# Optimization experiments

Measured on AMD Instinct MI355X. Metric: run time of the kernel, lower is better.

## Reference

```python
import jax, jax.numpy as jnp
import numpy as np

N_NODES = 100000
N_EDGES = 3200000
D_IN, D_HID, D_OUT = 256, 256, 256
B, V, C = 64, 50, 64
DEC_H1, DEC_H2, N_CLS = 512, 256, 1000
NEG_INF = -1e9


def setup_inputs() -> dict:
    key = jax.random.key(0)
    ks = jax.random.split(key, 20)
    s = lambda d: 1.0 / np.sqrt(d)
    return {
        'edge_index': jax.random.randint(ks[0], (2, N_EDGES), 0, N_NODES, dtype=jnp.int64 if jax.config.jax_enable_x64 else jnp.int32),
        'edge_weight': jax.random.uniform(ks[1], (N_EDGES,), dtype=jnp.float32),
        'codes_x': jax.random.randint(ks[2], (B, V, C), 0, N_NODES, dtype=jnp.int64 if jax.config.jax_enable_x64 else jnp.int32),
        'node_emb': jax.random.normal(ks[3], (N_NODES, D_IN), jnp.float32) * 0.02,
        'W1': jax.random.normal(ks[4], (D_IN, D_HID), jnp.float32) * s(D_IN),
        'b1': jnp.zeros((D_HID,), jnp.float32),
        'W2': jax.random.normal(ks[5], (D_HID, D_OUT), jnp.float32) * s(D_HID),
        'b2': jnp.zeros((D_OUT,), jnp.float32),
        'Wv': jax.random.normal(ks[6], (D_OUT, D_OUT), jnp.float32) * s(D_OUT),
        'uv': jax.random.normal(ks[7], (D_OUT,), jnp.float32) * s(D_OUT),
        'Wp': jax.random.normal(ks[8], (D_OUT, D_OUT), jnp.float32) * s(D_OUT),
        'up': jax.random.normal(ks[9], (D_OUT,), jnp.float32) * s(D_OUT),
        'Wd1': jax.random.normal(ks[10], (D_OUT, DEC_H1), jnp.float32) * s(D_OUT),
        'bd1': jnp.zeros((DEC_H1,), jnp.float32),
        'Wd2': jax.random.normal(ks[11], (DEC_H1, DEC_H2), jnp.float32) * s(DEC_H1),
        'bd2': jnp.zeros((DEC_H2,), jnp.float32),
        'Wd3': jax.random.normal(ks[12], (DEC_H2, N_CLS), jnp.float32) * s(DEC_H2),
        'bd3': jnp.zeros((N_CLS,), jnp.float32),
    }


def reference(edge_index, edge_weight, codes_x, node_emb, W1, b1, W2, b2,
              Wv, uv, Wp, up, Wd1, bd1, Wd2, bd2, Wd3, bd3):
    n = node_emb.shape[0]
    src, dst = edge_index[0], edge_index[1]

    def agg(x):  # weighted message passing: out_i = sum_{e: dst=i} w_e * x[src_e]
        return jax.ops.segment_sum(x[src] * edge_weight[:, None], dst, num_segments=n)

    # 2-layer weighted GCN over the code ontology graph (dropout in eval mode)
    h = jax.nn.relu(agg(node_emb) @ W1 + b1)          # [N, D_hid]
    emb = agg(h) @ W2 + b2                             # [N, D_out]

    # Ragged per-visit code attention, vectorized with masks (code id 0 = padding)
    code_mask = codes_x > 0                            # [B, V, C]
    ce = emb[codes_x]                                  # [B, V, C, D]
    ev = jnp.tanh(jnp.einsum('bvcd,de->bvce', ce, Wv)) @ uv   # [B, V, C]
    av = jax.nn.softmax(jnp.where(code_mask, ev, NEG_INF), axis=-1)
    vemb = jnp.einsum('bvc,bvcd->bvd', av, ce)         # [B, V, D]
    visit_mask = code_mask.any(-1)                     # [B, V]
    vemb = jnp.where(visit_mask[..., None], vemb, 0.0)

    # Per-patient visit attention over valid visits only
    ep = jnp.tanh(vemb @ Wp) @ up                      # [B, V]
    ap = jax.nn.softmax(jnp.where(visit_mask, ep, NEG_INF), axis=-1)
    pemb = jnp.einsum('bv,bvd->bd', ap, vemb)          # [B, D]
    pemb = jnp.where(visit_mask.any(-1)[:, None], pemb, 0.0)  # empty patient -> zeros

    # Decoder MLP classifier (train_type='direct')
    h1 = jax.nn.relu(pemb @ Wd1 + bd1)
    h2 = jax.nn.relu(h1 @ Wd2 + bd2)
    return h2 @ Wd3 + bd3                              # [B, n_classes]
```

## Files before the change

### kernel.cpp

```cpp
#include <hip/hip_runtime.h>
#include <hip/hip_bf16.h>
#include <math.h>


#define D 256
#define BPAT 64
#define VIS 50
#define CODES 64
#define NEG_INF -1e9f
#define MPAD 100096
#define BINB 32
#define NBIN 3125
#define SORTCAP 1536

typedef unsigned short ushort_t;
typedef short short8 __attribute__((ext_vector_type(8)));
typedef float f32x4 __attribute__((ext_vector_type(4)));

__device__ __forceinline__ float blo(unsigned u) { return __uint_as_float(u << 16); }
__device__ __forceinline__ float bhi(unsigned u) { return __uint_as_float(u & 0xffff0000u); }
__device__ __forceinline__ float bf2f(ushort_t u) { return __uint_as_float((unsigned)u << 16); }
__device__ __forceinline__ ushort_t f2bfu(float f) {
    __hip_bfloat16 h = __float2bfloat16(f);
    return *reinterpret_cast<ushort_t*>(&h);
}
__device__ __forceinline__ unsigned pack2(float a, float b) {
    return (unsigned)f2bfu(a) | ((unsigned)f2bfu(b) << 16);
}

__global__ __launch_bounds__(512) void count_transpose_kernel(
    const int* __restrict__ ei, int* __restrict__ bincount, int ne,
    const float* __restrict__ Wa, const float* __restrict__ Wb,
    const float* __restrict__ Wc, const float* __restrict__ Wd,
    ushort_t* __restrict__ Ta, ushort_t* __restrict__ Tb,
    ushort_t* __restrict__ Tc, ushort_t* __restrict__ Td) {
    __shared__ int h[NBIN];
    __shared__ float tt[2][32][33];
    if (blockIdx.x < 256) {
        for (int i = threadIdx.x; i < NBIN; i += 512) h[i] = 0;
        __syncthreads();
        const int stride = 256 * 512;
        for (int e = blockIdx.x * 512 + threadIdx.x; e < ne; e += stride)
            atomicAdd(&h[ei[(size_t)ne + e] >> 5], 1);
        __syncthreads();
        for (int i = threadIdx.x; i < NBIN; i += 512) {
            int c = h[i];
            if (c) atomicAdd(&bincount[i], c);
        }
    } else {
        int tile = (blockIdx.x - 256) * 2 + (threadIdx.x >> 8);
        int which = tile >> 6, rem = tile & 63;
        int bx = (rem & 7) << 5, by = (rem >> 3) << 5;
        const float* W = (which == 0) ? Wa : (which == 1) ? Wb
                        : (which == 2) ? Wc : Wd;
        ushort_t* Wt = (which == 0) ? Ta : (which == 1) ? Tb
                      : (which == 2) ? Tc : Td;
        int hf = threadIdx.x >> 8;
        int ltid = threadIdx.x & 255;
        int lx = ltid & 31, ly = ltid >> 5;
        #pragma unroll
        for (int i = 0; i < 32; i += 8)
            tt[hf][ly + i][lx] = W[(size_t)(by + ly + i) * 256 + bx + lx];
        __syncthreads();
        #pragma unroll
        for (int i = 0; i < 32; i += 8)
            Wt[(size_t)(bx + ly + i) * 256 + by + lx] = f2bfu(tt[hf][lx][ly + i]);
    }
}

__global__ __launch_bounds__(64) void bin_scan_kernel(
    const int* __restrict__ bincount, int* __restrict__ binstart,
    int* __restrict__ bincursor, int* __restrict__ rp, int ne, int nn) {
    __shared__ int carry;
    int lane = threadIdx.x;
    if (lane == 0) carry = 0;
    __syncthreads();
    for (int base = 0; base < NBIN; base += 64) {
        int i = base + lane;
        int v = (i < NBIN) ? bincount[i] : 0;
        int x = v;
        #pragma unroll
        for (int d = 1; d < 64; d <<= 1) {
            int y = __shfl_up(x, (unsigned)d, 64);
            if (lane >= d) x += y;
        }
        int c = carry;
        if (i < NBIN) { int ex = c + x - v; binstart[i] = ex; bincursor[i] = ex; }
        __syncthreads();
        if (lane == 63) carry = c + x;
        __syncthreads();
    }
    if (lane == 0) { binstart[NBIN] = ne; rp[nn] = ne; }
}

__global__ __launch_bounds__(512) void partition_kernel(
    const int* __restrict__ ei, const float* __restrict__ ew,
    int* __restrict__ bincursor, uint2* __restrict__ ptmp, int ne) {
    __shared__ int h[NBIN];
    __shared__ int base_[NBIN];
    for (int i = threadIdx.x; i < NBIN; i += 512) h[i] = 0;
    __syncthreads();
    int stride = gridDim.x * 512;
    for (int e = blockIdx.x * 512 + threadIdx.x; e < ne; e += stride)
        atomicAdd(&h[ei[(size_t)ne + e] >> 5], 1);
    __syncthreads();
    for (int i = threadIdx.x; i < NBIN; i += 512) {
        int c = h[i];
        base_[i] = c ? atomicAdd(&bincursor[i], c) : 0;
        h[i] = 0;
    }
    __syncthreads();
    for (int e = blockIdx.x * 512 + threadIdx.x; e < ne; e += stride) {
        int dd = ei[(size_t)ne + e];
        int ss = ei[e];
        float w = ew[e];
        int bin = dd >> 5;
        int r = atomicAdd(&h[bin], 1);
        ptmp[base_[bin] + r] =
            make_uint2((unsigned)ss | ((unsigned)(dd & 31) << 17),
                       __float_as_uint(w));
    }
}

__global__ __launch_bounds__(256) void binsort_kernel(
    const uint2* __restrict__ ptmp, const int* __restrict__ binstart,
    uint2* __restrict__ epair, int* __restrict__ rp) {
    int b = blockIdx.x;
    int tid = threadIdx.x;
    int beg = binstart[b], end = binstart[b + 1];
    int nE = end - beg;
    __shared__ uint2 sbuf[SORTCAP];
    __shared__ int cnt[BINB];
    __shared__ int cur[BINB];
    if (tid < BINB) cnt[tid] = 0;
    __syncthreads();
    if (nE <= SORTCAP) {
        for (int i = tid; i < nE; i += 256) {
            uint2 p = ptmp[beg + i];
            sbuf[i] = p;
            atomicAdd(&cnt[(p.x >> 17) & 31], 1);
        }
        __syncthreads();
        if (tid < BINB) {
            int v = cnt[tid];
            int x = v;
            #pragma unroll
            for (int d = 1; d < BINB; d <<= 1) {
                int y = __shfl_up(x, (unsigned)d, BINB);
                if (tid >= d) x += y;
            }
            int start = beg + x - v;
            cur[tid] = start;
            rp[b * BINB + tid] = start;
        }
        __syncthreads();
        for (int i = tid; i < nE; i += 256) {
            uint2 p = sbuf[i];
            int dl = (p.x >> 17) & 31;
            int pos = atomicAdd(&cur[dl], 1);
            epair[pos] = make_uint2(p.x & 0x1FFFF, p.y);
        }
    } else {
        for (int i = beg + tid; i < end; i += 256)
            atomicAdd(&cnt[(ptmp[i].x >> 17) & 31], 1);
        __syncthreads();
        if (tid < BINB) {
            int v = cnt[tid];
            int x = v;
            #pragma unroll
            for (int d = 1; d < BINB; d <<= 1) {
                int y = __shfl_up(x, (unsigned)d, BINB);
                if (tid >= d) x += y;
            }
            int start = beg + x - v;
            cur[tid] = start;
            rp[b * BINB + tid] = start;
        }
        __syncthreads();
        for (int i = beg + tid; i < end; i += 256) {
            uint2 p = ptmp[i];
            int dl = (p.x >> 17) & 31;
            int pos = atomicAdd(&cur[dl], 1);
            epair[pos] = make_uint2(p.x & 0x1FFFF, p.y);
        }
    }
}

__device__ __forceinline__ void acc8(float* a, uint4 v, float w) {
    a[0] += w * blo(v.x); a[1] += w * bhi(v.x);
    a[2] += w * blo(v.y); a[3] += w * bhi(v.y);
    a[4] += w * blo(v.z); a[5] += w * bhi(v.z);
    a[6] += w * blo(v.w); a[7] += w * bhi(v.w);
}

template<int ACT>
__global__ __launch_bounds__(256) void agg_bf16_kernel(
    const ushort_t* __restrict__ x, const int* __restrict__ rp,
    const uint2* __restrict__ ep, const float* __restrict__ bias,
    ushort_t* __restrict__ out, int n) {
    int wv = (int)(((size_t)blockIdx.x * blockDim.x + threadIdx.x) >> 6);
    int lane = threadIdx.x & 63;
    if (wv >= n) return;
    int half = lane >> 5;
    int l32 = lane & 31;
    int beg = rp[wv], end = rp[wv + 1];
    float a[8] = {};
    int e = beg;
    for (; e + 16 <= end; e += 16) {
        uint2 p0 = ep[e + half];
        uint2 p1 = ep[e + 2 + half];
        uint2 p2 = ep[e + 4 + half];
        uint2 p3 = ep[e + 6 + half];
        uint2 p4 = ep[e + 8 + half];
        uint2 p5 = ep[e + 10 + half];
        uint2 p6 = ep[e + 12 + half];
        uint2 p7 = ep[e + 14 + half];
        uint4 v0 = ((const uint4*)(x + (size_t)p0.x * D))[l32];
        uint4 v1 = ((const uint4*)(x + (size_t)p1.x * D))[l32];
        uint4 v2 = ((const uint4*)(x + (size_t)p2.x * D))[l32];
        uint4 v3 = ((const uint4*)(x + (size_t)p3.x * D))[l32];
        uint4 v4 = ((const uint4*)(x + (size_t)p4.x * D))[l32];
        uint4 v5 = ((const uint4*)(x + (size_t)p5.x * D))[l32];
        uint4 v6 = ((const uint4*)(x + (size_t)p6.x * D))[l32];
        uint4 v7 = ((const uint4*)(x + (size_t)p7.x * D))[l32];
        acc8(a, v0, __uint_as_float(p0.y));
        acc8(a, v1, __uint_as_float(p1.y));
        acc8(a, v2, __uint_as_float(p2.y));
        acc8(a, v3, __uint_as_float(p3.y));
        acc8(a, v4, __uint_as_float(p4.y));
        acc8(a, v5, __uint_as_float(p5.y));
        acc8(a, v6, __uint_as_float(p6.y));
        acc8(a, v7, __uint_as_float(p7.y));
    }
    for (; e + 4 <= end; e += 4) {
        uint2 p0 = ep[e + half];
        uint2 p1 = ep[e + 2 + half];
        uint4 v0 = ((const uint4*)(x + (size_t)p0.x * D))[l32];
        uint4 v1 = ((const uint4*)(x + (size_t)p1.x * D))[l32];
        acc8(a, v0, __uint_as_float(p0.y));
        acc8(a, v1, __uint_as_float(p1.y));
    }
    for (; e + 2 <= end; e += 2) {
        uint2 p0 = ep[e + half];
        uint4 v0 = ((const uint4*)(x + (size_t)p0.x * D))[l32];
        acc8(a, v0, __uint_as_float(p0.y));
    }
    if (e < end) {
        uint2 p0 = ep[e];
        uint4 v0 = ((const uint4*)(x + (size_t)p0.x * D))[l32];
        acc8(a, v0, half ? 0.f : __uint_as_float(p0.y));
    }
    #pragma unroll
    for (int j = 0; j < 8; ++j) a[j] += __shfl_xor(a[j], 32, 64);
    if (half == 0) {
        float4 b0 = ((const float4*)bias)[l32 * 2];
        float4 b1 = ((const float4*)bias)[l32 * 2 + 1];
        a[0] += b0.x; a[1] += b0.y; a[2] += b0.z; a[3] += b0.w;
        a[4] += b1.x; a[5] += b1.y; a[6] += b1.z; a[7] += b1.w;
        if (ACT == 1) {
            #pragma unroll
            for (int j = 0; j < 8; ++j) a[j] = fmaxf(a[j], 0.f);
        }
        uint4 o;
        o.x = pack2(a[0], a[1]); o.y = pack2(a[2], a[3]);
        o.z = pack2(a[4], a[5]); o.w = pack2(a[6], a[7]);
        ((uint4*)(out + (size_t)wv * D))[l32] = o;
    }
}

__global__ __launch_bounds__(512) void gemm_f32a_kernel(
    const float* __restrict__ Af, const ushort_t* __restrict__ Wt,
    ushort_t* __restrict__ out, int nvalid) {
    __shared__ __align__(16) ushort_t As[128 * 32];
    __shared__ __align__(16) ushort_t Bs[256 * 32];
    const int tid = threadIdx.x;
    const int lane = tid & 63;
    const int wv = tid >> 6;
    const int wr = wv >> 2, wc = wv & 3;
    const size_t brow = (size_t)blockIdx.x * 128;

    const int ra = tid >> 2, ca = tid & 3;
    const int rb1 = ra + 128;
    const int csa = ca ^ ((ra >> 1) & 3);
    const int arow = (int)brow + ra;
    const bool aval = arow < nvalid;
    const float* gAf = Af + (size_t)arow * 256 + ca * 8;
    const ushort_t* gB0 = Wt + (size_t)ra  * 256 + ca * 8;
    const ushort_t* gB1 = Wt + (size_t)rb1 * 256 + ca * 8;
    ushort_t* lA  = As + ra * 32 + csa * 8;
    ushort_t* lB0 = Bs + ra * 32 + csa * 8;
    ushort_t* lB1 = Bs + rb1 * 32 + csa * 8;

    const int g = lane >> 4, rl = lane & 15;
    int aoff[4], boff[4];
    #pragma unroll
    for (int m = 0; m < 4; ++m) {
        int row = wr * 64 + m * 16 + rl;
        aoff[m] = row * 32 + (g ^ ((row >> 1) & 3)) * 8;
    }
    #pragma unroll
    for (int n = 0; n < 4; ++n) {
        int row = wc * 64 + n * 16 + rl;
        boff[n] = row * 32 + (g ^ ((row >> 1) & 3)) * 8;
    }

    f32x4 acc[4][4] = {};
    float4 pa0 = make_float4(0.f, 0.f, 0.f, 0.f), pa1 = pa0;
    if (aval) { pa0 = *(const float4*)gAf; pa1 = *(const float4*)(gAf + 4); }
    uint4 vb0 = *(const uint4*)gB0;
    uint4 vb1 = *(const uint4*)gB1;

    for (int ks = 0; ks < 8; ++ks) {
        uint4 va;
        va.x = pack2(pa0.x, pa0.y); va.y = pack2(pa0.z, pa0.w);
        va.z = pack2(pa1.x, pa1.y); va.w = pack2(pa1.z, pa1.w);
        *(uint4*)lA = va; *(uint4*)lB0 = vb0; *(uint4*)lB1 = vb1;
        __syncthreads();
        if (ks < 7) {
            int k0 = (ks + 1) * 32;
            if (aval) {
                pa0 = *(const float4*)(gAf + k0);
                pa1 = *(const float4*)(gAf + k0 + 4);
            }
            vb0 = *(const uint4*)(gB0 + k0);
            vb1 = *(const uint4*)(gB1 + k0);
        }
        short8 af[4], bfv[4];
        #pragma unroll
        for (int m = 0; m < 4; ++m) af[m] = *(const short8*)(As + aoff[m]);
        #pragma unroll
        for (int n = 0; n < 4; ++n) bfv[n] = *(const short8*)(Bs + boff[n]);
        #pragma unroll
        for (int m = 0; m < 4; ++m)
            #pragma unroll
            for (int n = 0; n < 4; ++n)
                acc[m][n] = __builtin_amdgcn_mfma_f32_16x16x32_bf16(
                    af[m], bfv[n], acc[m][n], 0, 0, 0);
        __syncthreads();
    }

    #pragma unroll
    for (int m = 0; m < 4; ++m) {
        #pragma unroll
        for (int r = 0; r < 4; ++r) {
            size_t row = brow + wr * 64 + m * 16 + g * 4 + r;
            #pragma unroll
            for (int n = 0; n < 4; ++n) {
                int col = wc * 64 + n * 16 + rl;
                out[row * 256 + col] = f2bfu(acc[m][n][r]);
            }
        }
    }
}

template<int MODE>
__global__ __launch_bounds__(512) void mfma_gemm_kernel(
    const ushort_t* __restrict__ A, const ushort_t* __restrict__ Wt,
    const float* __restrict__ bias, ushort_t* __restrict__ out,
    const float* __restrict__ u, float* __restrict__ tout, int mvalid) {
    __shared__ __align__(16) ushort_t As[128 * 32];
    __shared__ __align__(16) ushort_t Bs[256 * 32];
    __shared__ float s_t[128];
    const int tid = threadIdx.x;
    const int lane = tid & 63;
    const int wv = tid >> 6;
    const int wr = wv >> 2, wc = wv & 3;
    const size_t brow = (size_t)blockIdx.x * 128;

    const int ra = tid >> 2, ca = tid & 3;
    const int rb1 = ra + 128;
    const int csa = ca ^ ((ra >> 1) & 3);
    const ushort_t* gA  = A  + (brow + ra) * 256 + ca * 8;
    const ushort_t* gB0 = Wt + (size_t)ra  * 256 + ca * 8;
    const ushort_t* gB1 = Wt + (size_t)rb1 * 256 + ca * 8;
    ushort_t* lA  = As + ra * 32 + csa * 8;
    ushort_t* lB0 = Bs + ra * 32 + csa * 8;
    ushort_t* lB1 = Bs + rb1 * 32 + csa * 8;

    const int g = lane >> 4, rl = lane & 15;
    int aoff[4], boff[4];
    #pragma unroll
    for (int m = 0; m < 4; ++m) {
        int row = wr * 64 + m * 16 + rl;
        aoff[m] = row * 32 + (g ^ ((row >> 1) & 3)) * 8;
    }
    #pragma unroll
    for (int n = 0; n < 4; ++n) {
        int row = wc * 64 + n * 16 + rl;
        boff[n] = row * 32 + (g ^ ((row >> 1) & 3)) * 8;
    }

    if (MODE == 2 && tid < 128) s_t[tid] = 0.f;

    f32x4 acc[4][4] = {};
    uint4 va  = *(const uint4*)gA;
    uint4 vb0 = *(const uint4*)gB0;
    uint4 vb1 = *(const uint4*)gB1;

    for (int ks = 0; ks < 8; ++ks) {
        *(uint4*)lA = va; *(uint4*)lB0 = vb0; *(uint4*)lB1 = vb1;
        __syncthreads();
        if (ks < 7) {
            int k0 = (ks + 1) * 32;
            va  = *(const uint4*)(gA + k0);
            vb0 = *(const uint4*)(gB0 + k0);
            vb1 = *(const uint4*)(gB1 + k0);
        }
        short8 af[4], bfv[4];
        #pragma unroll
        for (int m = 0; m < 4; ++m) af[m] = *(const short8*)(As + aoff[m]);
        #pragma unroll
        for (int n = 0; n < 4; ++n) bfv[n] = *(const short8*)(Bs + boff[n]);
        #pragma unroll
        for (int m = 0; m < 4; ++m)
            #pragma unroll
            for (int n = 0; n < 4; ++n)
                acc[m][n] = __builtin_amdgcn_mfma_f32_16x16x32_bf16(
                    af[m], bfv[n], acc[m][n], 0, 0, 0);
        __syncthreads();
    }

    if (MODE == 2) {
        float uvv[4];
        #pragma unroll
        for (int n = 0; n < 4; ++n) uvv[n] = u[wc * 64 + n * 16 + rl];
        #pragma unroll
        for (int m = 0; m < 4; ++m) {
            #pragma unroll
            for (int r = 0; r < 4; ++r) {
                float v = 0.f;
                #pragma unroll
                for (int n = 0; n < 4; ++n) v += tanhf(acc[m][n][r]) * uvv[n];
                v += __shfl_xor(v, 1, 64);
                v += __shfl_xor(v, 2, 64);
                v += __shfl_xor(v, 4, 64);
                v += __shfl_xor(v, 8, 64);
                if (rl == 0) atomicAdd(&s_t[wr * 64 + m * 16 + g * 4 + r], v);
            }
        }
        __syncthreads();
        if (tid < 128 && brow + tid < (size_t)mvalid) tout[brow + tid] = s_t[tid];
    } else {
        #pragma unroll
        for (int m = 0; m < 4; ++m) {
            #pragma unroll
            for (int r = 0; r < 4; ++r) {
                size_t row = brow + wr * 64 + m * 16 + g * 4 + r;
                #pragma unroll
                for (int n = 0; n < 4; ++n) {
                    int col = wc * 64 + n * 16 + rl;
                    float v = acc[m][n][r] + (bias ? bias[col] : 0.f);
                    out[row * 256 + col] = f2bfu(v);
                }
            }
        }
    }
}

__global__ __launch_bounds__(256) void code_attn_kernel(
    const int* __restrict__ codes, const float* __restrict__ t,
    const ushort_t* __restrict__ emb, ushort_t* __restrict__ vembB,
    int* __restrict__ vmask) {
    int bv = blockIdx.x;
    int tid = threadIdx.x;
    __shared__ int s_codes[CODES];
    __shared__ float s_av[CODES];
    __shared__ int s_valid;
    if (tid < 64) {
        int c = codes[(size_t)bv * CODES + tid];
        s_codes[tid] = c;
        float e = (c > 0) ? t[c] : NEG_INF;
        float m = e;
        #pragma unroll
        for (int d = 32; d; d >>= 1) m = fmaxf(m, __shfl_xor(m, d, 64));
        float ex = expf(e - m);
        float s = ex;
        #pragma unroll
        for (int d = 32; d; d >>= 1) s += __shfl_xor(s, d, 64);
        s_av[tid] = ex / s;
        if (tid == 0) s_valid = (m > -1e8f) ? 1 : 0;
    }
    __syncthreads();
    float acc = 0.f;
    #pragma unroll 8
    for (int c = 0; c < CODES; ++c)
        acc += s_av[c] * bf2f(emb[(size_t)s_codes[c] * D + tid]);
    int valid = s_valid;
    vembB[(size_t)bv * D + tid] = f2bfu(valid ? acc : 0.f);
    if (tid == 0) vmask[bv] = valid;
}

__global__ __launch_bounds__(512) void patient_dec_kernel(
    const ushort_t* __restrict__ vembB, const float* __restrict__ epr,
    const int* __restrict__ vmask,
    const float* __restrict__ Wd1, const float* __restrict__ bd1,
    const float* __restrict__ Wd2, const float* __restrict__ bd2,
    const float* __restrict__ Wd3, const float* __restrict__ bd3,
    float* __restrict__ outp) {
    int b = blockIdx.x;
    int tid = threadIdx.x;
    __shared__ float s_ap[VIS];
    __shared__ float s_x[256];
    __shared__ float s_h1[512];
    __shared__ float s_h2[256];
    __shared__ int s_any;

    if (tid < 64) {
        float e = -3e38f;
        if (tid < VIS) e = vmask[b * VIS + tid] ? epr[b * VIS + tid] : NEG_INF;
        float m = e;
        #pragma unroll
        for (int d = 32; d; d >>= 1) m = fmaxf(m, __shfl_xor(m, d, 64));
        float ex = (tid < VIS) ? expf(e - m) : 0.f;
        float s = ex;
        #pragma unroll
        for (int d = 32; d; d >>= 1) s += __shfl_xor(s, d, 64);
        if (tid < VIS) s_ap[tid] = ex / s;
        if (tid == 0) s_any = (m > -1e8f) ? 1 : 0;
    }
    __syncthreads();
    if (tid < 256) {
        float acc = 0.f;
        for (int v = 0; v < VIS; ++v)
            acc += s_ap[v] * bf2f(vembB[((size_t)b * VIS + v) * D + tid]);
        s_x[tid] = s_any ? acc : 0.f;
    }
    __syncthreads();
    {
        float acc = bd1[tid];
        #pragma unroll 8
        for (int k = 0; k < 256; ++k)
            acc = fmaf(s_x[k], Wd1[(size_t)k * 512 + tid], acc);
        s_h1[tid] = fmaxf(acc, 0.f);
    }
    __syncthreads();
    if (tid < 256) {
        float acc = bd2[tid];
        #pragma unroll 8
        for (int k = 0; k < 512; ++k)
            acc = fmaf(s_h1[k], Wd2[(size_t)k * 256 + tid], acc);
        s_h2[tid] = fmaxf(acc, 0.f);
    }
    __syncthreads();
    for (int j = tid; j < 1000; j += 512) {
        float acc = bd3[j];
        #pragma unroll 8
        for (int k = 0; k < 256; ++k)
            acc = fmaf(s_h2[k], Wd3[(size_t)k * 1000 + j], acc);
        outp[(size_t)b * 1000 + j] = acc;
    }
}

extern "C" void kernel_launch(void* const* d_in, const int* in_sizes, int n_in,
                              void* d_out, int out_size, void* d_ws, size_t ws_size,
                              hipStream_t stream) {
    const int* edge_index    = (const int*)d_in[0];
    const float* edge_weight = (const float*)d_in[1];
    const int* codes         = (const int*)d_in[2];
    const float* node_emb    = (const float*)d_in[3];
    const float* W1 = (const float*)d_in[4];
    const float* b1 = (const float*)d_in[5];
    const float* W2 = (const float*)d_in[6];
    const float* b2 = (const float*)d_in[7];
    const float* Wv = (const float*)d_in[8];
    const float* uv = (const float*)d_in[9];
    const float* Wp = (const float*)d_in[10];
    const float* up = (const float*)d_in[11];
    const float* Wd1 = (const float*)d_in[12];
    const float* bd1 = (const float*)d_in[13];
    const float* Wd2 = (const float*)d_in[14];
    const float* bd2 = (const float*)d_in[15];
    const float* Wd3 = (const float*)d_in[16];
    const float* bd3 = (const float*)d_in[17];

    const int NE = in_sizes[1];
    const int NN = in_sizes[3] / D;

    char* ws = (char*)d_ws;
    size_t off = 0;
    auto alloc = [&](size_t bytes) -> void* {
        void* p = ws + off;
        off += (bytes + 255) & ~(size_t)255;
        return p;
    };
    ushort_t* zbuf = (ushort_t*)alloc((size_t)MPAD * D * 2);
    ushort_t* hbuf = (ushort_t*)alloc((size_t)MPAD * D * 2);
    ushort_t* embB = (ushort_t*)alloc((size_t)MPAD * D * 2);
    uint2* ptmp   = (uint2*)alloc((size_t)NE * 8);
    uint2* epair  = (uint2*)alloc((size_t)NE * 8);
    int* bincount = (int*)alloc((size_t)NBIN * 4);
    int* binstart = (int*)alloc((size_t)(NBIN + 1) * 4);
    int* bincursor= (int*)alloc((size_t)NBIN * 4);
    int* rp       = (int*)alloc((size_t)(NN + 1) * 4);
    ushort_t* W1t = (ushort_t*)alloc(256 * 256 * 2);
    ushort_t* W2t = (ushort_t*)alloc(256 * 256 * 2);
    ushort_t* Wvt = (ushort_t*)alloc(256 * 256 * 2);
    ushort_t* Wpt = (ushort_t*)alloc(256 * 256 * 2);
    float* tbuf  = (float*)alloc((size_t)NN * 4);
    ushort_t* vembB = (ushort_t*)alloc((size_t)BPAT * VIS * D * 2);
    int*   vmask = (int*)  alloc((size_t)BPAT * VIS * 4);
    float* epr   = (float*)alloc((size_t)BPAT * VIS * 4);
    (void)ws_size; (void)n_in; (void)out_size;

    const int ab = NN / 4;

    hipMemsetAsync(bincount, 0, (size_t)NBIN * 4, stream);
    count_transpose_kernel<<<256 + 128, 512, 0, stream>>>(
        edge_index, bincount, NE, W1, W2, Wv, Wp, W1t, W2t, Wvt, Wpt);
    bin_scan_kernel<<<1, 64, 0, stream>>>(bincount, binstart, bincursor, rp, NE, NN);
    partition_kernel<<<256, 512, 0, stream>>>(edge_index, edge_weight,
                                              bincursor, ptmp, NE);
    binsort_kernel<<<NBIN, 256, 0, stream>>>(ptmp, binstart, epair, rp);

    gemm_f32a_kernel<<<MPAD / 128, 512, 0, stream>>>(node_emb, W1t, zbuf, NN);
    agg_bf16_kernel<1><<<ab, 256, 0, stream>>>(zbuf, rp, epair, b1, hbuf, NN);

    mfma_gemm_kernel<1><<<MPAD / 128, 512, 0, stream>>>(
        hbuf, W2t, nullptr, zbuf, nullptr, nullptr, 0);
    agg_bf16_kernel<0><<<ab, 256, 0, stream>>>(zbuf, rp, epair, b2, embB, NN);

    mfma_gemm_kernel<2><<<MPAD / 128, 512, 0, stream>>>(
        embB, Wvt, nullptr, nullptr, uv, tbuf, NN);

    code_attn_kernel<<<BPAT * VIS, 256, 0, stream>>>(codes, tbuf, embB, vembB, vmask);

    mfma_gemm_kernel<2><<<BPAT * VIS / 128, 512, 0, stream>>>(
        vembB, Wpt, nullptr, nullptr, up, epr, BPAT * VIS);

    patient_dec_kernel<<<BPAT, 512, 0, stream>>>(
        vembB, epr, vmask, Wd1, bd1, Wd2, bd2, Wd3, bd3, (float*)d_out);
}
```

Baseline: 802.7 us.

## Co-schedule edge partitioning with first GEMM in one launch; use fast tanh

Merges the edge partition kernel and the node_emb×W1 GEMM into a single launch. The first 256 blocks do partitioning and the remaining blocks do GEMM tiles, so the two independent stages overlap on the GPU and one launch is removed. It also replaces tanhf with an exp-based fast tanh in the attention-score GEMM epilogue. Risks: the shared memory footprint of both paths is combined, which raises per-block LDS use and may lower occupancy. The fast tanh is slightly less accurate.

```diff
diff --git a/kernel.cpp b/kernel.cpp
--- a/kernel.cpp
+++ b/kernel.cpp
@@ -26,6 +26,9 @@
 }
 __device__ __forceinline__ unsigned pack2(float a, float b) {
     return (unsigned)f2bfu(a) | ((unsigned)f2bfu(b) << 16);
+}
+__device__ __forceinline__ float fast_tanh(float x) {
+    return 1.f - 2.f / (__expf(2.f * x) + 1.f);
 }
 
 __global__ __launch_bounds__(512) void count_transpose_kernel(
@@ -93,32 +96,118 @@
     if (lane == 0) { binstart[NBIN] = ne; rp[nn] = ne; }
 }
 
-__global__ __launch_bounds__(512) void partition_kernel(
+__global__ __launch_bounds__(512) void part_gemm_kernel(
     const int* __restrict__ ei, const float* __restrict__ ew,
-    int* __restrict__ bincursor, uint2* __restrict__ ptmp, int ne) {
+    int* __restrict__ bincursor, uint2* __restrict__ ptmp, int ne,
+    const float* __restrict__ Af, const ushort_t* __restrict__ Wt,
+    ushort_t* __restrict__ out, int nvalid) {
     __shared__ int h[NBIN];
     __shared__ int base_[NBIN];
-    for (int i = threadIdx.x; i < NBIN; i += 512) h[i] = 0;
-    __syncthreads();
-    int stride = gridDim.x * 512;
-    for (int e = blockIdx.x * 512 + threadIdx.x; e < ne; e += stride)
-        atomicAdd(&h[ei[(size_t)ne + e] >> 5], 1);
-    __syncthreads();
-    for (int i = threadIdx.x; i < NBIN; i += 512) {
-        int c = h[i];
-        base_[i] = c ? atomicAdd(&bincursor[i], c) : 0;
-        h[i] = 0;
-    }
-    __syncthreads();
-    for (int e = blockIdx.x * 512 + threadIdx.x; e < ne; e += stride) {
-        int dd = ei[(size_t)ne + e];
-        int ss = ei[e];
-        float w = ew[e];
-        int bin = dd >> 5;
-        int r = atomicAdd(&h[bin], 1);
-        ptmp[base_[bin] + r] =
-            make_uint2((unsigned)ss | ((unsigned)(dd & 31) << 17),
-                       __float_as_uint(w));
+    __shared__ __align__(16) ushort_t As[128 * 32];
+    __shared__ __align__(16) ushort_t Bs[256 * 32];
+    const int tid = threadIdx.x;
+    if (blockIdx.x < 256) {
+        for (int i = tid; i < NBIN; i += 512) h[i] = 0;
+        __syncthreads();
+        const int stride = 256 * 512;
+        for (int e = blockIdx.x * 512 + tid; e < ne; e += stride)
+            atomicAdd(&h[ei[(size_t)ne + e] >> 5], 1);
+        __syncthreads();
+        for (int i = tid; i < NBIN; i += 512) {
+            int c = h[i];
+            base_[i] = c ? atomicAdd(&bincursor[i], c) : 0;
+            h[i] = 0;
+        }
+        __syncthreads();
+        for (int e = blockIdx.x * 512 + tid; e < ne; e += stride) {
+            int dd = ei[(size_t)ne + e];
+            int ss = ei[e];
+            float w = ew[e];
+            int bin = dd >> 5;
+            int r = atomicAdd(&h[bin], 1);
+            ptmp[base_[bin] + r] =
+                make_uint2((unsigned)ss | ((unsigned)(dd & 31) << 17),
+                           __float_as_uint(w));
+        }
+        return;
+    }
+    const int gbid = blockIdx.x - 256;
+    const int lane = tid & 63;
+    const int wv = tid >> 6;
+    const int wr = wv >> 2, wc = wv & 3;
+    const size_t brow = (size_t)gbid * 128;
+
+    const int ra = tid >> 2, ca = tid & 3;
+    const int rb1 = ra + 128;
+    const int csa = ca ^ ((ra >> 1) & 3);
+    const int arow = (int)brow + ra;
+    const bool aval = arow < nvalid;
+    const float* gAf = Af + (size_t)arow * 256 + ca * 8;
+    const ushort_t* gB0 = Wt + (size_t)ra  * 256 + ca * 8;
+    const ushort_t* gB1 = Wt + (size_t)rb1 * 256 + ca * 8;
+    ushort_t* lA  = As + ra * 32 + csa * 8;
+    ushort_t* lB0 = Bs + ra * 32 + csa * 8;
+    ushort_t* lB1 = Bs + rb1 * 32 + csa * 8;
+
+    const int g = lane >> 4, rl = lane & 15;
+    int aoff[4], boff[4];
+    #pragma unroll
+    for (int m = 0; m < 4; ++m) {
+        int row = wr * 64 + m * 16 + rl;
+        aoff[m] = row * 32 + (g ^ ((row >> 1) & 3)) * 8;
+    }
+    #pragma unroll
+    for (int n = 0; n < 4; ++n) {
+        int row = wc * 64 + n * 16 + rl;
+        boff[n] = row * 32 + (g ^ ((row >> 1) & 3)) * 8;
+    }
+
+    f32x4 acc[4][4] = {};
+    float4 pa0 = make_float4(0.f, 0.f, 0.f, 0.f), pa1 = pa0;
+    if (aval) { pa0 = *(const float4*)gAf; pa1 = *(const float4*)(gAf + 4); }
+    uint4 vb0 = *(const uint4*)gB0;
+    uint4 vb1 = *(const uint4*)gB1;
+
+    for (int ks = 0; ks < 8; ++ks) {
+        uint4 va;
+        va.x = pack2(pa0.x, pa0.y); va.y = pack2(pa0.z, pa0.w);
+        va.z = pack2(pa1.x, pa1.y); va.w = pack2(pa1.z, pa1.w);
+        *(uint4*)lA = va; *(uint4*)lB0 = vb0; *(uint4*)lB1 = vb1;
+        __syncthreads();
+        if (ks < 7) {
+            int k0 = (ks + 1) * 32;
+            if (aval) {
+                pa0 = *(const float4*)(gAf + k0);
+                pa1 = *(const float4*)(gAf + k0 + 4);
+            }
+            vb0 = *(const uint4*)(gB0 + k0);
+            vb1 = *(const uint4*)(gB1 + k0);
+        }
+        short8 af[4], bfv[4];
+        #pragma unroll
+        for (int m = 0; m < 4; ++m) af[m] = *(const short8*)(As + aoff[m]);
+        #pragma unroll
+        for (int n = 0; n < 4; ++n) bfv[n] = *(const short8*)(Bs + boff[n]);
+        #pragma unroll
+        for (int m = 0; m < 4; ++m)
+            #pragma unroll
+            for (int n = 0; n < 4; ++n)
+                acc[m][n] = __builtin_amdgcn_mfma_f32_16x16x32_bf16(
+                    af[m], bfv[n], acc[m][n], 0, 0, 0);
+        __syncthreads();
+    }
+
+    #pragma unroll
+    for (int m = 0; m < 4; ++m) {
+        #pragma unroll
+        for (int r = 0; r < 4; ++r) {
+            size_t row = brow + wr * 64 + m * 16 + g * 4 + r;
+            #pragma unroll
+            for (int n = 0; n < 4; ++n) {
+                int col = wc * 64 + n * 16 + rl;
+                out[row * 256 + col] = f2bfu(acc[m][n][r]);
+            }
+        }
     }
 }
 
@@ -268,91 +357,6 @@
     }
 }
 
-__global__ __launch_bounds__(512) void gemm_f32a_kernel(
-    const float* __restrict__ Af, const ushort_t* __restrict__ Wt,
-    ushort_t* __restrict__ out, int nvalid) {
-    __shared__ __align__(16) ushort_t As[128 * 32];
-    __shared__ __align__(16) ushort_t Bs[256 * 32];
-    const int tid = threadIdx.x;
-    const int lane = tid & 63;
-    const int wv = tid >> 6;
-    const int wr = wv >> 2, wc = wv & 3;
-    const size_t brow = (size_t)blockIdx.x * 128;
-
-    const int ra = tid >> 2, ca = tid & 3;
-    const int rb1 = ra + 128;
-    const int csa = ca ^ ((ra >> 1) & 3);
-    const int arow = (int)brow + ra;
-    const bool aval = arow < nvalid;
-    const float* gAf = Af + (size_t)arow * 256 + ca * 8;
-    const ushort_t* gB0 = Wt + (size_t)ra  * 256 + ca * 8;
-    const ushort_t* gB1 = Wt + (size_t)rb1 * 256 + ca * 8;
-    ushort_t* lA  = As + ra * 32 + csa * 8;
-    ushort_t* lB0 = Bs + ra * 32 + csa * 8;
-    ushort_t* lB1 = Bs + rb1 * 32 + csa * 8;
-
-    const int g = lane >> 4, rl = lane & 15;
-    int aoff[4], boff[4];
-    #pragma unroll
-    for (int m = 0; m < 4; ++m) {
-        int row = wr * 64 + m * 16 + rl;
-        aoff[m] = row * 32 + (g ^ ((row >> 1) & 3)) * 8;
-    }
-    #pragma unroll
-    for (int n = 0; n < 4; ++n) {
-        int row = wc * 64 + n * 16 + rl;
-        boff[n] = row * 32 + (g ^ ((row >> 1) & 3)) * 8;
-    }
-
-    f32x4 acc[4][4] = {};
-    float4 pa0 = make_float4(0.f, 0.f, 0.f, 0.f), pa1 = pa0;
-    if (aval) { pa0 = *(const float4*)gAf; pa1 = *(const float4*)(gAf + 4); }
-    uint4 vb0 = *(const uint4*)gB0;
-    uint4 vb1 = *(const uint4*)gB1;
-
-    for (int ks = 0; ks < 8; ++ks) {
-        uint4 va;
-        va.x = pack2(pa0.x, pa0.y); va.y = pack2(pa0.z, pa0.w);
-        va.z = pack2(pa1.x, pa1.y); va.w = pack2(pa1.z, pa1.w);
-        *(uint4*)lA = va; *(uint4*)lB0 = vb0; *(uint4*)lB1 = vb1;
-        __syncthreads();
-        if (ks < 7) {
-            int k0 = (ks + 1) * 32;
-            if (aval) {
-                pa0 = *(const float4*)(gAf + k0);
-                pa1 = *(const float4*)(gAf + k0 + 4);
-            }
-            vb0 = *(const uint4*)(gB0 + k0);
-            vb1 = *(const uint4*)(gB1 + k0);
-        }
-        short8 af[4], bfv[4];
-        #pragma unroll
-        for (int m = 0; m < 4; ++m) af[m] = *(const short8*)(As + aoff[m]);
-        #pragma unroll
-        for (int n = 0; n < 4; ++n) bfv[n] = *(const short8*)(Bs + boff[n]);
-        #pragma unroll
-        for (int m = 0; m < 4; ++m)
-            #pragma unroll
-            for (int n = 0; n < 4; ++n)
-                acc[m][n] = __builtin_amdgcn_mfma_f32_16x16x32_bf16(
-                    af[m], bfv[n], acc[m][n], 0, 0, 0);
-        __syncthreads();
-    }
-
-    #pragma unroll
-    for (int m = 0; m < 4; ++m) {
-        #pragma unroll
-        for (int r = 0; r < 4; ++r) {
-            size_t row = brow + wr * 64 + m * 16 + g * 4 + r;
-            #pragma unroll
-            for (int n = 0; n < 4; ++n) {
-                int col = wc * 64 + n * 16 + rl;
-                out[row * 256 + col] = f2bfu(acc[m][n][r]);
-            }
-        }
-    }
-}
-
 template<int MODE>
 __global__ __launch_bounds__(512) void mfma_gemm_kernel(
     const ushort_t* __restrict__ A, const ushort_t* __restrict__ Wt,
@@ -430,7 +434,7 @@
             for (int r = 0; r < 4; ++r) {
                 float v = 0.f;
                 #pragma unroll
-                for (int n = 0; n < 4; ++n) v += tanhf(acc[m][n][r]) * uvv[n];
+                for (int n = 0; n < 4; ++n) v += fast_tanh(acc[m][n][r]) * uvv[n];
                 v += __shfl_xor(v, 1, 64);
                 v += __shfl_xor(v, 2, 64);
                 v += __shfl_xor(v, 4, 64);
@@ -608,11 +612,11 @@
     count_transpose_kernel<<<256 + 128, 512, 0, stream>>>(
         edge_index, bincount, NE, W1, W2, Wv, Wp, W1t, W2t, Wvt, Wpt);
     bin_scan_kernel<<<1, 64, 0, stream>>>(bincount, binstart, bincursor, rp, NE, NN);
-    partition_kernel<<<256, 512, 0, stream>>>(edge_index, edge_weight,
-                                              bincursor, ptmp, NE);
+    part_gemm_kernel<<<256 + MPAD / 128, 512, 0, stream>>>(
+        edge_index, edge_weight, bincursor, ptmp, NE,
+        node_emb, W1t, zbuf, NN);
     binsort_kernel<<<NBIN, 256, 0, stream>>>(ptmp, binstart, epair, rp);
 
-    gemm_f32a_kernel<<<MPAD / 128, 512, 0, stream>>>(node_emb, W1t, zbuf, NN);
     agg_bf16_kernel<1><<<ab, 256, 0, stream>>>(zbuf, rp, epair, b1, hbuf, NN);
 
     mfma_gemm_kernel<1><<<MPAD / 128, 512, 0, stream>>>(
```

Result: no change. 794.6 us, median of 2 (-1.0%).
